# Kernel tuning notes

Measured on AMD Instinct MI355X. Metric: run time of the kernel, lower is better.

Reference implementation:

```python
import jax, jax.numpy as jnp
import numpy as np

D = 256          # object_dim == query_dim
HG = 1024        # g hidden / output width
HF0, HF1 = 1024, 512
OUT_F = 256
N = 32768        # number of objects


def _mlp_g(h, W0, b0, W1, b1, W2, b2):
    # g=True: ReLU after every layer, including output.
    h = jax.nn.relu(h @ W0 + b0)
    h = jax.nn.relu(h @ W1 + b1)
    return jax.nn.relu(h @ W2 + b2)


def _mlp_f(h, W0, b0, W1, b1, W2, b2):
    # f: ReLU on hidden layers, linear output.
    h = jax.nn.relu(h @ W0 + b0)
    h = jax.nn.relu(h @ W1 + b1)
    return h @ W2 + b2


def setup_inputs() -> dict:
    key = jax.random.key(0)
    ks = jax.random.split(key, 16)
    def lin(k, fan_in, fan_out):
        s = 1.0 / np.sqrt(fan_in)
        kw, kb = jax.random.split(k)
        W = jax.random.uniform(kw, (fan_in, fan_out), jnp.float32, -s, s)
        b = jax.random.uniform(kb, (fan_out,), jnp.float32, -s, s)
        return W, b
    x = jax.random.normal(ks[0], (N, D), jnp.float32)
    q = jax.random.normal(ks[1], (D,), jnp.float32)
    g_W0, g_b0 = lin(ks[2], 3 * D, HG)
    g_W1, g_b1 = lin(ks[3], HG, HG)
    g_W2, g_b2 = lin(ks[4], HG, HG)
    f_W0, f_b0 = lin(ks[5], HG, HF0)
    f_W1, f_b1 = lin(ks[6], HF0, HF1)
    f_W2, f_b2 = lin(ks[7], HF1, OUT_F)
    return dict(x=x, q=q,
                g_W0=g_W0, g_b0=g_b0, g_W1=g_W1, g_b1=g_b1, g_W2=g_W2, g_b2=g_b2,
                f_W0=f_W0, f_b0=f_b0, f_W1=f_W1, f_b1=f_b1, f_W2=f_W2, f_b2=f_b2)


def reference(x, q, g_W0, g_b0, g_W1, g_b1, g_W2, g_b2,
              f_W0, f_b0, f_W1, f_b1, f_W2, f_b2):
    n = x.shape[0]
    # mode 4: adjacent pairs (o_i, o_{i+1}), query concatenated to each pair.
    pair_concat = jnp.concatenate(
        [x[:-1], x[1:], jnp.broadcast_to(q, (n - 1, q.shape[0]))], axis=-1)  # (n-1, 3D)
    relations = _mlp_g(pair_concat, g_W0, g_b0, g_W1, g_b1, g_W2, g_b2)       # (n-1, HG)
    embedding = jnp.sum(relations, axis=0)                                     # (HG,)
    return _mlp_f(embedding, f_W0, f_b0, f_W1, f_b1, f_W2, f_b2)               # (OUT_F,)
```

## Files before the change

kernel.cpp:

```cpp
#include <hip/hip_runtime.h>

typedef __attribute__((ext_vector_type(8))) short short8;
typedef __attribute__((ext_vector_type(4))) float floatx4;
typedef __attribute__((ext_vector_type(4))) unsigned int uint32x4;

#define NROWS 32768L
#define NVALID 32767L
#define HGDIM 1024

__device__ __forceinline__ unsigned short f2bf_rne(float f) {
    union { float f; unsigned u; } v; v.f = f;
    unsigned r = v.u + 0x7fffu + ((v.u >> 16) & 1u);
    return (unsigned short)(r >> 16);
}

__device__ __forceinline__ void gload_lds16(const void* g, void* l) {
    __builtin_amdgcn_global_load_lds(
        (const __attribute__((address_space(1))) void*)g,
        (__attribute__((address_space(3))) void*)l,
        16, 0, 0);
}

#define NB_CVT 8193
#define NB_T0  512
#define NB_T1  1024
#define NB_T2  1024
#define NB_C0  4

__global__ void prep(const float* __restrict__ x, unsigned short* __restrict__ xb,
                     const float* __restrict__ gW0, unsigned short* __restrict__ w0t,
                     const float* __restrict__ gW1, unsigned short* __restrict__ w1t,
                     const float* __restrict__ gW2, unsigned short* __restrict__ w2t,
                     const float* __restrict__ q, const float* __restrict__ gb0,
                     float* __restrict__ c0, float* __restrict__ emb,
                     float* __restrict__ e1, float* __restrict__ e2,
                     float* __restrict__ out) {
    __shared__ float smem[1056];
    int b = blockIdx.x, tid = threadIdx.x;
    if (b < NB_CVT) {
        long i = (long)b * 256 + tid;
        long ntot4 = (NROWS + 1) * 64;
        if (i < ntot4) {
            long i4 = i * 4, nx = NROWS * 256;
            float4 v = make_float4(0.f, 0.f, 0.f, 0.f);
            if (i4 < nx) v = *(const float4*)(x + i4);
            ushort4 o;
            o.x = f2bf_rne(v.x); o.y = f2bf_rne(v.y);
            o.z = f2bf_rne(v.z); o.w = f2bf_rne(v.w);
            *(ushort4*)(xb + i4) = o;
        }
        return;
    }
    b -= NB_CVT;
    const float* W; unsigned short* Wt; int K, N;
    if (b < NB_T0)                  { W = gW0; Wt = w0t; K = 512;  N = 1024; }
    else if (b < NB_T0 + NB_T1)     { b -= NB_T0; W = gW1; Wt = w1t; K = 1024; N = 1024; }
    else if (b < NB_T0 + NB_T1 + NB_T2) { b -= NB_T0 + NB_T1; W = gW2; Wt = w2t; K = 1024; N = 1024; }
    else if (b < NB_T0 + NB_T1 + NB_T2 + NB_C0) {
        b -= NB_T0 + NB_T1 + NB_T2;
        int j = b * 256 + tid;
        smem[tid] = q[tid];
        __syncthreads();
        float a = gb0[j];
        #pragma unroll 4
        for (int k = 0; k < 256; ++k)
            a += smem[k] * gW0[(size_t)(512 + k) * 1024 + j];
        c0[j] = a;
        return;
    } else {
        for (int i = tid; i < 1024; i += 256) { emb[i] = 0.f; e1[i] = 0.f; e2[i] = 0.f; }
        if (tid < 256) out[tid] = 0.f;
        return;
    }
    int bx = b & 31, by = b >> 5;
    float (*tile)[33] = (float(*)[33])smem;
    int tx = tid & 31, ty = tid >> 5;
    int nb2 = bx * 32, kb = by * 32;
    #pragma unroll
    for (int i = 0; i < 32; i += 8)
        tile[ty + i][tx] = W[(size_t)(kb + ty + i) * N + (nb2 + tx)];
    __syncthreads();
    #pragma unroll
    for (int i = 0; i < 32; i += 8)
        Wt[(size_t)(nb2 + ty + i) * K + (kb + tx)] = f2bf_rne(tile[tx][ty + i]);
}

template<bool RELU_IN>
__global__ void fc_partial(const float* __restrict__ in, const float* __restrict__ W,
                           const float* __restrict__ bias, float* __restrict__ out,
                           int N) {
    __shared__ float s_in[128];
    int j = blockIdx.x * 256 + threadIdx.x;
    int k0 = blockIdx.y * 128;
    if (threadIdx.x < 128) {
        float v = in[k0 + threadIdx.x];
        if (RELU_IN) v = fmaxf(v, 0.f);
        s_in[threadIdx.x] = v;
    }
    __syncthreads();
    float acc = (blockIdx.y == 0) ? bias[j] : 0.f;
    #pragma unroll 4
    for (int k = 0; k < 128; ++k)
        acc += s_in[k] * W[(size_t)(k0 + k) * N + j];
    atomicAdd(&out[j], acc);
}


#define SBAR() __builtin_amdgcn_sched_barrier(0)

#define U_PRE() do { SBAR(); \
    asm volatile("s_waitcnt lgkmcnt(0)" ::: "memory"); SBAR(); \
    __builtin_amdgcn_s_setprio(1); } while (0)

#define U_POST() do { __builtin_amdgcn_s_setprio(0); SBAR(); \
    asm volatile("s_waitcnt vmcnt(2)" ::: "memory"); SBAR(); \
    __builtin_amdgcn_s_barrier(); } while (0)

#define STAGE(buf, region, T) do { \
    if ((region) >= 2) { \
        const unsigned short* _g = gA + (long)(((region) & 1) * 128) * lda + (long)(T) * 64; \
        char* _d = (char*)&lds[buf][0][((region) & 1) * 128][0] + t * 16; \
        gload_lds16(_g, _d); \
        gload_lds16(_g + 64L * lda, _d + 8192); \
    } else { \
        const unsigned short* _g = gB + (long)(((region) & 1) * 128) * ldb + (long)(T) * 64; \
        char* _d = (char*)&lds[buf][1][((region) & 1) * 128][0] + t * 16; \
        gload_lds16(_g, _d); \
        gload_lds16(_g + 64L * ldb, _d + 8192); \
    } } while (0)

#define LDA4(dst, buf, mbase, ks) do { _Pragma("unroll") for (int _q = 0; _q < 4; ++_q) \
    dst[_q] = *(const short8*)((const char*)&lds[buf][0][arowb + ((mbase) + _q) * 16][0] + ((ks) ? cb1 : cb0)); } while (0)

#define LDB4(dst, buf, ks) do { _Pragma("unroll") for (int _q = 0; _q < 4; ++_q) \
    dst[_q] = *(const short8*)((const char*)&lds[buf][1][browb + _q * 16][0] + ((ks) ? cb1 : cb0)); } while (0)

#define MFMA16(AF, BF, MO) do { _Pragma("unroll") for (int _mf = 0; _mf < 4; ++_mf) { \
    _Pragma("unroll") for (int _nf = 0; _nf < 4; ++_nf) \
        acc[(MO) + _mf][_nf] = __builtin_amdgcn_mfma_f32_16x16x32_bf16(AF[_mf], BF[_nf], acc[(MO) + _mf][_nf], 0, 0, 0); } } while (0)

template<int COLSUM>
__global__ __launch_bounds__(512, 2)
void gemmU(const unsigned short* __restrict__ A, int lda,
           const unsigned short* __restrict__ Bt, int ldb,
           const float* __restrict__ bias, int K,
           unsigned short* __restrict__ Hout,
           float* __restrict__ emb, long row0g, long nvalid,
           int mblocks) {
    __shared__ alignas(16) unsigned short lds[2][2][256][64];

    const int t = threadIdx.x;
    int nwg = gridDim.x, bid = blockIdx.x, swz;
    if ((nwg & 7) == 0) { int cpx = nwg >> 3; swz = (bid & 7) * cpx + (bid >> 3); }
    else swz = bid;
    const int mb = swz >> 2, nb = swz & 3;
    const long m0 = (long)mb * 256;
    const int n0 = nb * 256;

    const int srow = t >> 3;
    const int ssc = (t & 7) ^ (srow & 7);
    const unsigned short* gA = A + (m0 + srow) * (long)lda + ssc * 8;
    const unsigned short* gB = Bt + ((long)n0 + srow) * (long)ldb + ssc * 8;

    const int lane = t & 63;
    const int wv = t >> 6;
    const int wm = wv >> 2, wn = wv & 3;
    const int arowb = wm * 128 + (lane & 15);
    const int browb = wn * 64 + (lane & 15);
    const int c0x = (lane >> 4) ^ (lane & 7);
    const int cb0 = c0x * 16;
    const int cb1 = (c0x ^ 4) * 16;

    floatx4 acc[8][4] = {};

    const int NT = K >> 6;
    const int NI = NT >> 1;

    short8 bE0[4], bE1[4], bO0[4], bO1[4];
    short8 aE0[4], aE1[4], aE2[4], aE3[4], aO0[4], aO1[4], aO2[4], aO3[4];

    STAGE(0, 0, 0); STAGE(0, 1, 0); STAGE(0, 2, 0); STAGE(0, 3, 0);
    STAGE(1, 0, 1); STAGE(1, 1, 1);
    asm volatile("s_waitcnt vmcnt(4)" ::: "memory");
    SBAR();
    __builtin_amdgcn_s_barrier();
    SBAR();
    LDB4(bE0, 0, 0); LDA4(aE0, 0, 0, 0);

    for (int i = 0; i < NI; ++i) {
        const int O = 2 * i + 1;
        int N2 = 2 * i + 2; if (N2 >= NT) N2 = 0;
        int P2 = 2 * i + 3; if (P2 >= NT) P2 = 1;

        U_PRE();
        LDA4(aE1, 0, 4, 0);
        STAGE(1, 2, O);
        MFMA16(aE0, bE0, 0);
        U_POST();
        U_PRE();
        LDB4(bE1, 0, 1); LDA4(aE2, 0, 0, 1);
        STAGE(1, 3, O);
        MFMA16(aE1, bE0, 4);
        U_POST();
        U_PRE();
        LDA4(aE3, 0, 4, 1);
        STAGE(0, 0, N2);
        MFMA16(aE2, bE1, 0);
        U_POST();
        U_PRE();
        LDB4(bO0, 1, 0); LDA4(aO0, 1, 0, 0);
        STAGE(0, 1, N2);
        MFMA16(aE3, bE1, 4);
        U_POST();
        U_PRE();
        LDA4(aO1, 1, 4, 0);
        STAGE(0, 2, N2);
        MFMA16(aO0, bO0, 0);
        U_POST();
        U_PRE();
        LDB4(bO1, 1, 1); LDA4(aO2, 1, 0, 1);
        STAGE(0, 3, N2);
        MFMA16(aO1, bO0, 4);
        U_POST();
        U_PRE();
        LDA4(aO3, 1, 4, 1);
        STAGE(1, 0, P2);
        MFMA16(aO2, bO1, 0);
        U_POST();
        U_PRE();
        LDB4(bE0, 0, 0); LDA4(aE0, 0, 0, 0);
        STAGE(1, 1, P2);
        MFMA16(aO3, bO1, 4);
        U_POST();
    }
    asm volatile("s_waitcnt vmcnt(0) lgkmcnt(0)" ::: "memory");
    SBAR();
    __builtin_amdgcn_s_barrier();

    if (COLSUM == 0) {
        char* slb = (char*)&lds[0][0][0][0];
        #pragma unroll
        for (int nf = 0; nf < 4; ++nf) {
            int ncol = wn * 64 + nf * 16 + (lane & 15);
            float bv = bias[n0 + ncol];
            #pragma unroll
            for (int mf = 0; mf < 8; ++mf) {
                int rbase = wm * 128 + mf * 16 + ((lane >> 4) << 2);
                #pragma unroll
                for (int j = 0; j < 4; ++j) {
                    int row = rbase + j;
                    float v = fmaxf(acc[mf][nf][j] + bv, 0.f);
                    int byte = row * 512 + ((ncol * 2) ^ ((row & 7) << 4));
                    *(unsigned short*)(slb + byte) = f2bf_rne(v);
                }
            }
        }
        __syncthreads();
        {
            int rsub = t >> 5;
            int cb = (t & 31) * 16;
            #pragma unroll
            for (int i2 = 0; i2 < 16; ++i2) {
                int row = i2 * 16 + rsub;
                const char* src = slb + row * 512 + (cb ^ ((row & 7) << 4));
                uint32x4 v = *(const uint32x4*)src;
                char* dst = (char*)Hout + ((size_t)(m0 + row) * HGDIM + n0) * 2 + cb;
                *(uint32x4*)dst = v;
            }
        }
    } else {
        #pragma unroll
        for (int nf = 0; nf < 4; ++nf) {
            int ncol = n0 + wn * 64 + nf * 16 + (lane & 15);
            float bv = bias[ncol];
            float cs = 0.f;
            #pragma unroll
            for (int mf = 0; mf < 8; ++mf) {
                long rbase = row0g + m0 + wm * 128 + mf * 16 + ((lane >> 4) << 2);
                #pragma unroll
                for (int j = 0; j < 4; ++j) {
                    float v = fmaxf(acc[mf][nf][j] + bv, 0.f);
                    if (rbase + j < nvalid) cs += v;
                }
            }
            cs += __shfl_xor(cs, 16);
            cs += __shfl_xor(cs, 32);
            if ((lane >> 4) == 0) atomicAdd(&emb[ncol], cs);
        }
    }
}

extern "C" void kernel_launch(void* const* d_in, const int* in_sizes, int n_in,
                              void* d_out, int out_size, void* d_ws, size_t ws_size,
                              hipStream_t stream) {
    const float* x   = (const float*)d_in[0];
    const float* q   = (const float*)d_in[1];
    const float* gW0 = (const float*)d_in[2];
    const float* gb0 = (const float*)d_in[3];
    const float* gW1 = (const float*)d_in[4];
    const float* gb1 = (const float*)d_in[5];
    const float* gW2 = (const float*)d_in[6];
    const float* gb2 = (const float*)d_in[7];
    const float* fW0 = (const float*)d_in[8];
    const float* fb0 = (const float*)d_in[9];
    const float* fW1 = (const float*)d_in[10];
    const float* fb1 = (const float*)d_in[11];
    const float* fW2 = (const float*)d_in[12];
    const float* fb2 = (const float*)d_in[13];
    float* out = (float*)d_out;

    char* ws = (char*)d_ws;
    size_t off = 0;
    auto alloc = [&](size_t bytes) -> char* {
        char* p = ws + off;
        off += (bytes + 255) & ~(size_t)255;
        return p;
    };
    unsigned short* xb  = (unsigned short*)alloc((NROWS + 1) * 256 * 2);
    unsigned short* w0t = (unsigned short*)alloc((size_t)1024 * 512 * 2);
    unsigned short* w1t = (unsigned short*)alloc((size_t)1024 * 1024 * 2);
    unsigned short* w2t = (unsigned short*)alloc((size_t)1024 * 1024 * 2);
    float* c0  = (float*)alloc(4096);
    float* emb = (float*)alloc(4096);
    float* e1  = (float*)alloc(4096);
    float* e2  = (float*)alloc(4096);
    size_t fixed = off;
    size_t avail = (ws_size > fixed) ? ws_size - fixed : 0;
    long CR = (long)((avail / 2) / (HGDIM * 2));
    CR = (CR / 512) * 512;
    if (CR > NROWS) CR = NROWS;
    if (CR < 512) CR = 512;
    unsigned short* H0 = (unsigned short*)alloc((size_t)CR * HGDIM * 2);
    unsigned short* H1 = (unsigned short*)alloc((size_t)CR * HGDIM * 2);

    prep<<<dim3(NB_CVT + NB_T0 + NB_T1 + NB_T2 + NB_C0 + 1), 256, 0, stream>>>(
        x, xb, gW0, w0t, gW1, w1t, gW2, w2t, q, gb0, c0, emb, e1, e2, out);

    for (long r0 = 0; r0 < NROWS; r0 += CR) {
        long rows = NROWS - r0; if (rows > CR) rows = CR;
        int mblocks = (int)(rows / 256);
        dim3 g((unsigned)(mblocks * 4));
        gemmU<0><<<g, 512, 0, stream>>>(xb + r0 * 256, 256, w0t, 512, c0, 512,
                                        H0, nullptr, 0, 0, mblocks);
        gemmU<0><<<g, 512, 0, stream>>>(H0, 1024, w1t, 1024, gb1, 1024,
                                        H1, nullptr, 0, 0, mblocks);
        gemmU<1><<<g, 512, 0, stream>>>(H1, 1024, w2t, 1024, gb2, 1024,
                                        nullptr, emb, r0, NVALID, mblocks);
    }

    fc_partial<false><<<dim3(4, 8), 256, 0, stream>>>(emb, fW0, fb0, e1, 1024);
    fc_partial<true><<<dim3(2, 8), 256, 0, stream>>>(e1, fW1, fb1, e2, 512);
    fc_partial<true><<<dim3(1, 4), 256, 0, stream>>>(e2, fW2, fb2, out, 256);
}
```

Measured before the change: 234.2 us.

## Fuse prep, three GEMMs and FC layers into one cooperative persistent kernel

Replaces the sequence of separate launches (prep, three GEMMs, three FC kernels) with a single cooperative kernel of 256 workgroups. Phases are separated by grid.sync, and each workgroup processes two 256-row tiles per GEMM stage. The aim is to remove launch gaps and kernel-boundary drains. In exchange, each GEMM phase runs exactly 256 workgroups, which may fill the CUs less evenly, and grid-wide barriers add their own cost. The fused path only runs when cooperative launch is supported and the workspace holds all rows; otherwise the old multi-launch path is used.

```diff
diff --git a/kernel.cpp b/kernel.cpp
--- a/kernel.cpp
+++ b/kernel.cpp
@@ -1,4 +1,7 @@
 #include <hip/hip_runtime.h>
+#include <hip/hip_cooperative_groups.h>
+
+namespace cg = cooperative_groups;
 
 typedef __attribute__((ext_vector_type(8))) short short8;
 typedef __attribute__((ext_vector_type(4))) float floatx4;
@@ -19,6 +22,309 @@
         (const __attribute__((address_space(1))) void*)g,
         (__attribute__((address_space(3))) void*)l,
         16, 0, 0);
+}
+
+#define SBAR() __builtin_amdgcn_sched_barrier(0)
+
+#define U_PRE() do { SBAR(); \
+    asm volatile("s_waitcnt lgkmcnt(0)" ::: "memory"); SBAR(); \
+    __builtin_amdgcn_s_setprio(1); } while (0)
+
+#define U_POST() do { __builtin_amdgcn_s_setprio(0); SBAR(); \
+    asm volatile("s_waitcnt vmcnt(2)" ::: "memory"); SBAR(); \
+    __builtin_amdgcn_s_barrier(); } while (0)
+
+#define STAGE(buf, region, T) do { \
+    if ((region) >= 2) { \
+        const unsigned short* _g = gA + (long)(((region) & 1) * 128) * lda + (long)(T) * 64; \
+        char* _d = (char*)&lds[buf][0][((region) & 1) * 128][0] + t * 16; \
+        gload_lds16(_g, _d); \
+        gload_lds16(_g + 64L * lda, _d + 8192); \
+    } else { \
+        const unsigned short* _g = gB + (long)(((region) & 1) * 128) * ldb + (long)(T) * 64; \
+        char* _d = (char*)&lds[buf][1][((region) & 1) * 128][0] + t * 16; \
+        gload_lds16(_g, _d); \
+        gload_lds16(_g + 64L * ldb, _d + 8192); \
+    } } while (0)
+
+#define LDA4(dst, buf, mbase, ks) do { _Pragma("unroll") for (int _q = 0; _q < 4; ++_q) \
+    dst[_q] = *(const short8*)((const char*)&lds[buf][0][arowb + ((mbase) + _q) * 16][0] + ((ks) ? cb1 : cb0)); } while (0)
+
+#define LDB4(dst, buf, ks) do { _Pragma("unroll") for (int _q = 0; _q < 4; ++_q) \
+    dst[_q] = *(const short8*)((const char*)&lds[buf][1][browb + _q * 16][0] + ((ks) ? cb1 : cb0)); } while (0)
+
+#define MFMA16(AF, BF, MO) do { _Pragma("unroll") for (int _mf = 0; _mf < 4; ++_mf) { \
+    _Pragma("unroll") for (int _nf = 0; _nf < 4; ++_nf) \
+        acc[(MO) + _mf][_nf] = __builtin_amdgcn_mfma_f32_16x16x32_bf16(AF[_mf], BF[_nf], acc[(MO) + _mf][_nf], 0, 0, 0); } } while (0)
+
+template<int COLSUM>
+__device__ __forceinline__ void gemm_body(
+    unsigned short (&lds)[2][2][256][64],
+    const unsigned short* __restrict__ A, int lda,
+    const unsigned short* __restrict__ Bt, int ldb,
+    const float* __restrict__ bias, int K,
+    unsigned short* __restrict__ Hout, float* __restrict__ emb,
+    long row0g, long m0, int n0, long nvalid, int t)
+{
+    __syncthreads();
+
+    const int srow = t >> 3;
+    const int ssc = (t & 7) ^ (srow & 7);
+    const unsigned short* gA = A + (m0 + srow) * (long)lda + ssc * 8;
+    const unsigned short* gB = Bt + ((long)n0 + srow) * (long)ldb + ssc * 8;
+
+    const int lane = t & 63;
+    const int wv = t >> 6;
+    const int wm = wv >> 2, wn = wv & 3;
+    const int arowb = wm * 128 + (lane & 15);
+    const int browb = wn * 64 + (lane & 15);
+    const int c0x = (lane >> 4) ^ (lane & 7);
+    const int cb0 = c0x * 16;
+    const int cb1 = (c0x ^ 4) * 16;
+
+    floatx4 acc[8][4] = {};
+    const int NT = K >> 6;
+    const int NI = NT >> 1;
+
+    short8 bE0[4], bE1[4], bO0[4], bO1[4];
+    short8 aE0[4], aE1[4], aE2[4], aE3[4], aO0[4], aO1[4], aO2[4], aO3[4];
+
+    STAGE(0, 0, 0); STAGE(0, 1, 0); STAGE(0, 2, 0); STAGE(0, 3, 0);
+    STAGE(1, 0, 1); STAGE(1, 1, 1);
+    asm volatile("s_waitcnt vmcnt(4)" ::: "memory");
+    SBAR();
+    __builtin_amdgcn_s_barrier();
+    SBAR();
+    LDB4(bE0, 0, 0); LDA4(aE0, 0, 0, 0);
+
+    for (int i = 0; i < NI; ++i) {
+        const int O = 2 * i + 1;
+        int N2 = 2 * i + 2; if (N2 >= NT) N2 = 0;
+        int P2 = 2 * i + 3; if (P2 >= NT) P2 = 1;
+
+        U_PRE();
+        LDA4(aE1, 0, 4, 0);
+        STAGE(1, 2, O);
+        MFMA16(aE0, bE0, 0);
+        U_POST();
+        U_PRE();
+        LDB4(bE1, 0, 1); LDA4(aE2, 0, 0, 1);
+        STAGE(1, 3, O);
+        MFMA16(aE1, bE0, 4);
+        U_POST();
+        U_PRE();
+        LDA4(aE3, 0, 4, 1);
+        STAGE(0, 0, N2);
+        MFMA16(aE2, bE1, 0);
+        U_POST();
+        U_PRE();
+        LDB4(bO0, 1, 0); LDA4(aO0, 1, 0, 0);
+        STAGE(0, 1, N2);
+        MFMA16(aE3, bE1, 4);
+        U_POST();
+        U_PRE();
+        LDA4(aO1, 1, 4, 0);
+        STAGE(0, 2, N2);
+        MFMA16(aO0, bO0, 0);
+        U_POST();
+        U_PRE();
+        LDB4(bO1, 1, 1); LDA4(aO2, 1, 0, 1);
+        STAGE(0, 3, N2);
+        MFMA16(aO1, bO0, 4);
+        U_POST();
+        U_PRE();
+        LDA4(aO3, 1, 4, 1);
+        STAGE(1, 0, P2);
+        MFMA16(aO2, bO1, 0);
+        U_POST();
+        U_PRE();
+        LDB4(bE0, 0, 0); LDA4(aE0, 0, 0, 0);
+        STAGE(1, 1, P2);
+        MFMA16(aO3, bO1, 4);
+        U_POST();
+    }
+    asm volatile("s_waitcnt vmcnt(0) lgkmcnt(0)" ::: "memory");
+    SBAR();
+    __builtin_amdgcn_s_barrier();
+
+    if (COLSUM == 0) {
+        char* slb = (char*)&lds[0][0][0][0];
+        #pragma unroll
+        for (int nf = 0; nf < 4; ++nf) {
+            int ncol = wn * 64 + nf * 16 + (lane & 15);
+            float bv = bias[n0 + ncol];
+            #pragma unroll
+            for (int mf = 0; mf < 8; ++mf) {
+                int rbase = wm * 128 + mf * 16 + ((lane >> 4) << 2);
+                #pragma unroll
+                for (int j = 0; j < 4; ++j) {
+                    int row = rbase + j;
+                    float v = fmaxf(acc[mf][nf][j] + bv, 0.f);
+                    int byte = row * 512 + ((ncol * 2) ^ ((row & 7) << 4));
+                    *(unsigned short*)(slb + byte) = f2bf_rne(v);
+                }
+            }
+        }
+        __syncthreads();
+        {
+            int rsub = t >> 5;
+            int cb = (t & 31) * 16;
+            #pragma unroll
+            for (int i2 = 0; i2 < 16; ++i2) {
+                int row = i2 * 16 + rsub;
+                const char* src = slb + row * 512 + (cb ^ ((row & 7) << 4));
+                uint32x4 v = *(const uint32x4*)src;
+                char* dst = (char*)Hout + ((size_t)(m0 + row) * HGDIM + n0) * 2 + cb;
+                *(uint32x4*)dst = v;
+            }
+        }
+    } else {
+        #pragma unroll
+        for (int nf = 0; nf < 4; ++nf) {
+            int ncol = n0 + wn * 64 + nf * 16 + (lane & 15);
+            float bv = bias[ncol];
+            float cs = 0.f;
+            #pragma unroll
+            for (int mf = 0; mf < 8; ++mf) {
+                long rbase = row0g + m0 + wm * 128 + mf * 16 + ((lane >> 4) << 2);
+                #pragma unroll
+                for (int j = 0; j < 4; ++j) {
+                    float v = fmaxf(acc[mf][nf][j] + bv, 0.f);
+                    if (rbase + j < nvalid) cs += v;
+                }
+            }
+            cs += __shfl_xor(cs, 16);
+            cs += __shfl_xor(cs, 32);
+            if ((lane >> 4) == 0) atomicAdd(&emb[ncol], cs);
+        }
+    }
+}
+
+struct RNParams {
+    const float *x, *q, *gW0, *gb0, *gW1, *gb1, *gW2, *gb2;
+    const float *fW0, *fb0, *fW1, *fb1, *fW2, *fb2;
+    unsigned short *xb, *w0t, *w1t, *w2t;
+    float *c0, *emb, *e1, *e2;
+    unsigned short *H0, *H1;
+    float *outp;
+};
+
+__device__ __forceinline__ void fc_phase(bool relu_in, const float* in, const float* W,
+                                         const float* bias, float* out, int N, int ky,
+                                         int t, int bid, float* sbuf) {
+    int nx = N >> 8;
+    int njobs = nx * ky;
+    bool act = bid < njobs;
+    int bx = 0, by = 0;
+    if (act) { bx = bid % nx; by = bid / nx; }
+    if (act && t < 128) {
+        float v = in[by * 128 + t];
+        if (relu_in) v = fmaxf(v, 0.f);
+        sbuf[t] = v;
+    }
+    __syncthreads();
+    if (act && t < 256) {
+        int j = bx * 256 + t;
+        float a = (by == 0) ? bias[j] : 0.f;
+        #pragma unroll 4
+        for (int k = 0; k < 128; ++k)
+            a += sbuf[k] * W[(size_t)(by * 128 + k) * N + j];
+        atomicAdd(&out[j], a);
+    }
+    __syncthreads();
+}
+
+__global__ __launch_bounds__(512, 2) void fused_rn(RNParams p) {
+    __shared__ alignas(16) unsigned short lds[2][2][256][64];
+    cg::grid_group grid = cg::this_grid();
+    const int bid = blockIdx.x, t = threadIdx.x;
+
+    {
+        long ntot4 = (NROWS + 1) * 64;
+        long nx = NROWS * 256;
+        for (long i = (long)bid * 512 + t; i < ntot4; i += 131072) {
+            long i4 = i * 4;
+            float4 v = make_float4(0.f, 0.f, 0.f, 0.f);
+            if (i4 < nx) v = *(const float4*)(p.x + i4);
+            ushort4 o;
+            o.x = f2bf_rne(v.x); o.y = f2bf_rne(v.y);
+            o.z = f2bf_rne(v.z); o.w = f2bf_rne(v.w);
+            *(ushort4*)(p.xb + i4) = o;
+        }
+    }
+    {
+        float (*tiles)[32][33] = (float (*)[32][33])((void*)lds);
+        int half = t >> 8, ht = t & 255;
+        int tx = ht & 31, ty = ht >> 5;
+        for (int job = bid * 2 + half; job < 2560; job += 512) {
+            const float* W; unsigned short* Wt; int K, N; int jj = job;
+            if (jj < 512)       {             W = p.gW0; Wt = p.w0t; K = 512;  N = 1024; }
+            else if (jj < 1536) { jj -= 512;  W = p.gW1; Wt = p.w1t; K = 1024; N = 1024; }
+            else                { jj -= 1536; W = p.gW2; Wt = p.w2t; K = 1024; N = 1024; }
+            int bx = jj & 31, by = jj >> 5;
+            int nb2 = bx * 32, kb = by * 32;
+            #pragma unroll
+            for (int i = 0; i < 32; i += 8)
+                tiles[half][ty + i][tx] = W[(size_t)(kb + ty + i) * N + (nb2 + tx)];
+            __syncthreads();
+            #pragma unroll
+            for (int i = 0; i < 32; i += 8)
+                Wt[(size_t)(nb2 + ty + i) * K + (kb + tx)] = f2bf_rne(tiles[half][tx][ty + i]);
+            __syncthreads();
+        }
+    }
+    {
+        float* qs = (float*)lds;
+        if (bid < 4 && t < 256) qs[t] = p.q[t];
+        __syncthreads();
+        if (bid < 4 && t < 256) {
+            int j = bid * 256 + t;
+            float a = p.gb0[j];
+            #pragma unroll 4
+            for (int k = 0; k < 256; ++k)
+                a += qs[k] * p.gW0[(size_t)(512 + k) * 1024 + j];
+            p.c0[j] = a;
+        } else if (bid == 4) {
+            for (int i2 = t; i2 < 1024; i2 += 512) { p.emb[i2] = 0.f; p.e1[i2] = 0.f; p.e2[i2] = 0.f; }
+            if (t < 256) p.outp[t] = 0.f;
+        }
+    }
+    __threadfence();
+    grid.sync();
+
+    int swz = (bid & 7) * 32 + (bid >> 3);
+    const int mbB = swz >> 2, nb = swz & 3;
+    const long m0a = (long)mbB * 512;
+    const int n0 = nb * 256;
+
+    #pragma clang loop unroll(disable)
+    for (int s = 0; s < 2; ++s)
+        gemm_body<0>(lds, p.xb, 256, p.w0t, 512, p.c0, 512, p.H0, nullptr,
+                     0, m0a + s * 256, n0, 0, t);
+    __threadfence();
+    grid.sync();
+
+    #pragma clang loop unroll(disable)
+    for (int s = 0; s < 2; ++s)
+        gemm_body<0>(lds, p.H0, 1024, p.w1t, 1024, p.gb1, 1024, p.H1, nullptr,
+                     0, m0a + s * 256, n0, 0, t);
+    __threadfence();
+    grid.sync();
+
+    #pragma clang loop unroll(disable)
+    for (int s = 0; s < 2; ++s)
+        gemm_body<1>(lds, p.H1, 1024, p.w2t, 1024, p.gb2, 1024, nullptr, p.emb,
+                     0, m0a + s * 256, n0, NVALID, t);
+    __threadfence();
+    grid.sync();
+
+    fc_phase(false, p.emb, p.fW0, p.fb0, p.e1, 1024, 8, t, bid, (float*)lds);
+    __threadfence();
+    grid.sync();
+    fc_phase(true, p.e1, p.fW1, p.fb1, p.e2, 512, 8, t, bid, (float*)lds);
+    __threadfence();
+    grid.sync();
+    fc_phase(true, p.e2, p.fW2, p.fb2, p.outp, 256, 4, t, bid, (float*)lds);
 }
 
 #define NB_CVT 8193
@@ -105,189 +411,20 @@
     atomicAdd(&out[j], acc);
 }
 
-
-#define SBAR() __builtin_amdgcn_sched_barrier(0)
-
-#define U_PRE() do { SBAR(); \
-    asm volatile("s_waitcnt lgkmcnt(0)" ::: "memory"); SBAR(); \
-    __builtin_amdgcn_s_setprio(1); } while (0)
-
-#define U_POST() do { __builtin_amdgcn_s_setprio(0); SBAR(); \
-    asm volatile("s_waitcnt vmcnt(2)" ::: "memory"); SBAR(); \
-    __builtin_amdgcn_s_barrier(); } while (0)
-
-#define STAGE(buf, region, T) do { \
-    if ((region) >= 2) { \
-        const unsigned short* _g = gA + (long)(((region) & 1) * 128) * lda + (long)(T) * 64; \
-        char* _d = (char*)&lds[buf][0][((region) & 1) * 128][0] + t * 16; \
-        gload_lds16(_g, _d); \
-        gload_lds16(_g + 64L * lda, _d + 8192); \
-    } else { \
-        const unsigned short* _g = gB + (long)(((region) & 1) * 128) * ldb + (long)(T) * 64; \
-        char* _d = (char*)&lds[buf][1][((region) & 1) * 128][0] + t * 16; \
-        gload_lds16(_g, _d); \
-        gload_lds16(_g + 64L * ldb, _d + 8192); \
-    } } while (0)
-
-#define LDA4(dst, buf, mbase, ks) do { _Pragma("unroll") for (int _q = 0; _q < 4; ++_q) \
-    dst[_q] = *(const short8*)((const char*)&lds[buf][0][arowb + ((mbase) + _q) * 16][0] + ((ks) ? cb1 : cb0)); } while (0)
-
-#define LDB4(dst, buf, ks) do { _Pragma("unroll") for (int _q = 0; _q < 4; ++_q) \
-    dst[_q] = *(const short8*)((const char*)&lds[buf][1][browb + _q * 16][0] + ((ks) ? cb1 : cb0)); } while (0)
-
-#define MFMA16(AF, BF, MO) do { _Pragma("unroll") for (int _mf = 0; _mf < 4; ++_mf) { \
-    _Pragma("unroll") for (int _nf = 0; _nf < 4; ++_nf) \
-        acc[(MO) + _mf][_nf] = __builtin_amdgcn_mfma_f32_16x16x32_bf16(AF[_mf], BF[_nf], acc[(MO) + _mf][_nf], 0, 0, 0); } } while (0)
-
 template<int COLSUM>
 __global__ __launch_bounds__(512, 2)
-void gemmU(const unsigned short* __restrict__ A, int lda,
-           const unsigned short* __restrict__ Bt, int ldb,
-           const float* __restrict__ bias, int K,
-           unsigned short* __restrict__ Hout,
-           float* __restrict__ emb, long row0g, long nvalid,
-           int mblocks) {
+void gemm_k(const unsigned short* __restrict__ A, int lda,
+            const unsigned short* __restrict__ Bt, int ldb,
+            const float* __restrict__ bias, int K,
+            unsigned short* __restrict__ Hout, float* __restrict__ emb,
+            long row0g, long nvalid) {
     __shared__ alignas(16) unsigned short lds[2][2][256][64];
-
-    const int t = threadIdx.x;
     int nwg = gridDim.x, bid = blockIdx.x, swz;
     if ((nwg & 7) == 0) { int cpx = nwg >> 3; swz = (bid & 7) * cpx + (bid >> 3); }
     else swz = bid;
-    const int mb = swz >> 2, nb = swz & 3;
-    const long m0 = (long)mb * 256;
-    const int n0 = nb * 256;
-
-    const int srow = t >> 3;
-    const int ssc = (t & 7) ^ (srow & 7);
-    const unsigned short* gA = A + (m0 + srow) * (long)lda + ssc * 8;
-    const unsigned short* gB = Bt + ((long)n0 + srow) * (long)ldb + ssc * 8;
-
-    const int lane = t & 63;
-    const int wv = t >> 6;
-    const int wm = wv >> 2, wn = wv & 3;
-    const int arowb = wm * 128 + (lane & 15);
-    const int browb = wn * 64 + (lane & 15);
-    const int c0x = (lane >> 4) ^ (lane & 7);
-    const int cb0 = c0x * 16;
-    const int cb1 = (c0x ^ 4) * 16;
-
-    floatx4 acc[8][4] = {};
-
-    const int NT = K >> 6;
-    const int NI = NT >> 1;
-
-    short8 bE0[4], bE1[4], bO0[4], bO1[4];
-    short8 aE0[4], aE1[4], aE2[4], aE3[4], aO0[4], aO1[4], aO2[4], aO3[4];
-
-    STAGE(0, 0, 0); STAGE(0, 1, 0); STAGE(0, 2, 0); STAGE(0, 3, 0);
-    STAGE(1, 0, 1); STAGE(1, 1, 1);
-    asm volatile("s_waitcnt vmcnt(4)" ::: "memory");
-    SBAR();
-    __builtin_amdgcn_s_barrier();
-    SBAR();
-    LDB4(bE0, 0, 0); LDA4(aE0, 0, 0, 0);
-
-    for (int i = 0; i < NI; ++i) {
-        const int O = 2 * i + 1;
-        int N2 = 2 * i + 2; if (N2 >= NT) N2 = 0;
-        int P2 = 2 * i + 3; if (P2 >= NT) P2 = 1;
-
-        U_PRE();
-        LDA4(aE1, 0, 4, 0);
-        STAGE(1, 2, O);
-        MFMA16(aE0, bE0, 0);
-        U_POST();
-        U_PRE();
-        LDB4(bE1, 0, 1); LDA4(aE2, 0, 0, 1);
-        STAGE(1, 3, O);
-        MFMA16(aE1, bE0, 4);
-        U_POST();
-        U_PRE();
-        LDA4(aE3, 0, 4, 1);
-        STAGE(0, 0, N2);
-        MFMA16(aE2, bE1, 0);
-        U_POST();
-        U_PRE();
-        LDB4(bO0, 1, 0); LDA4(aO0, 1, 0, 0);
-        STAGE(0, 1, N2);
-        MFMA16(aE3, bE1, 4);
-        U_POST();
-        U_PRE();
-        LDA4(aO1, 1, 4, 0);
-        STAGE(0, 2, N2);
-        MFMA16(aO0, bO0, 0);
-        U_POST();
-        U_PRE();
-        LDB4(bO1, 1, 1); LDA4(aO2, 1, 0, 1);
-        STAGE(0, 3, N2);
-        MFMA16(aO1, bO0, 4);
-        U_POST();
-        U_PRE();
-        LDA4(aO3, 1, 4, 1);
-        STAGE(1, 0, P2);
-        MFMA16(aO2, bO1, 0);
-        U_POST();
-        U_PRE();
-        LDB4(bE0, 0, 0); LDA4(aE0, 0, 0, 0);
-        STAGE(1, 1, P2);
-        MFMA16(aO3, bO1, 4);
-        U_POST();
-    }
-    asm volatile("s_waitcnt vmcnt(0) lgkmcnt(0)" ::: "memory");
-    SBAR();
-    __builtin_amdgcn_s_barrier();
-
-    if (COLSUM == 0) {
-        char* slb = (char*)&lds[0][0][0][0];
-        #pragma unroll
-        for (int nf = 0; nf < 4; ++nf) {
-            int ncol = wn * 64 + nf * 16 + (lane & 15);
-            float bv = bias[n0 + ncol];
-            #pragma unroll
-            for (int mf = 0; mf < 8; ++mf) {
-                int rbase = wm * 128 + mf * 16 + ((lane >> 4) << 2);
-                #pragma unroll
-                for (int j = 0; j < 4; ++j) {
-                    int row = rbase + j;
-                    float v = fmaxf(acc[mf][nf][j] + bv, 0.f);
-                    int byte = row * 512 + ((ncol * 2) ^ ((row & 7) << 4));
-                    *(unsigned short*)(slb + byte) = f2bf_rne(v);
-                }
-            }
-        }
-        __syncthreads();
-        {
-            int rsub = t >> 5;
-            int cb = (t & 31) * 16;
-            #pragma unroll
-            for (int i2 = 0; i2 < 16; ++i2) {
-                int row = i2 * 16 + rsub;
-                const char* src = slb + row * 512 + (cb ^ ((row & 7) << 4));
-                uint32x4 v = *(const uint32x4*)src;
-                char* dst = (char*)Hout + ((size_t)(m0 + row) * HGDIM + n0) * 2 + cb;
-                *(uint32x4*)dst = v;
-            }
-        }
-    } else {
-        #pragma unroll
-        for (int nf = 0; nf < 4; ++nf) {
-            int ncol = n0 + wn * 64 + nf * 16 + (lane & 15);
-            float bv = bias[ncol];
-            float cs = 0.f;
-            #pragma unroll
-            for (int mf = 0; mf < 8; ++mf) {
-                long rbase = row0g + m0 + wm * 128 + mf * 16 + ((lane >> 4) << 2);
-                #pragma unroll
-                for (int j = 0; j < 4; ++j) {
-                    float v = fmaxf(acc[mf][nf][j] + bv, 0.f);
-                    if (rbase + j < nvalid) cs += v;
-                }
-            }
-            cs += __shfl_xor(cs, 16);
-            cs += __shfl_xor(cs, 32);
-            if ((lane >> 4) == 0) atomicAdd(&emb[ncol], cs);
-        }
-    }
+    int mb = swz >> 2, nb = swz & 3;
+    gemm_body<COLSUM>(lds, A, lda, Bt, ldb, bias, K, Hout, emb,
+                      row0g, (long)mb * 256, nb * 256, nvalid, threadIdx.x);
 }
 
 extern "C" void kernel_launch(void* const* d_in, const int* in_sizes, int n_in,
@@ -333,22 +470,38 @@
     unsigned short* H0 = (unsigned short*)alloc((size_t)CR * HGDIM * 2);
     unsigned short* H1 = (unsigned short*)alloc((size_t)CR * HGDIM * 2);
 
-    prep<<<dim3(NB_CVT + NB_T0 + NB_T1 + NB_T2 + NB_C0 + 1), 256, 0, stream>>>(
-        x, xb, gW0, w0t, gW1, w1t, gW2, w2t, q, gb0, c0, emb, e1, e2, out);
-
-    for (long r0 = 0; r0 < NROWS; r0 += CR) {
-        long rows = NROWS - r0; if (rows > CR) rows = CR;
-        int mblocks = (int)(rows / 256);
-        dim3 g((unsigned)(mblocks * 4));
-        gemmU<0><<<g, 512, 0, stream>>>(xb + r0 * 256, 256, w0t, 512, c0, 512,
-                                        H0, nullptr, 0, 0, mblocks);
-        gemmU<0><<<g, 512, 0, stream>>>(H0, 1024, w1t, 1024, gb1, 1024,
-                                        H1, nullptr, 0, 0, mblocks);
-        gemmU<1><<<g, 512, 0, stream>>>(H1, 1024, w2t, 1024, gb2, 1024,
-                                        nullptr, emb, r0, NVALID, mblocks);
-    }
-
-    fc_partial<false><<<dim3(4, 8), 256, 0, stream>>>(emb, fW0, fb0, e1, 1024);
-    fc_partial<true><<<dim3(2, 8), 256, 0, stream>>>(e1, fW1, fb1, e2, 512);
-    fc_partial<true><<<dim3(1, 4), 256, 0, stream>>>(e2, fW2, fb2, out, 256);
-}
+    int dev = 0;
+    hipGetDevice(&dev);
+    int coop = 0;
+    hipDeviceGetAttribute(&coop, hipDeviceAttributeCooperativeLaunch, dev);
+
+    if (coop && CR >= NROWS) {
+        RNParams p;
+        p.x = x; p.q = q; p.gW0 = gW0; p.gb0 = gb0; p.gW1 = gW1; p.gb1 = gb1;
+        p.gW2 = gW2; p.gb2 = gb2; p.fW0 = fW0; p.fb0 = fb0; p.fW1 = fW1; p.fb1 = fb1;
+        p.fW2 = fW2; p.fb2 = fb2; p.xb = xb; p.w0t = w0t; p.w1t = w1t; p.w2t = w2t;
+        p.c0 = c0; p.emb = emb; p.e1 = e1; p.e2 = e2; p.H0 = H0; p.H1 = H1; p.outp = out;
+        void* kargs[] = { (void*)&p };
+        hipLaunchCooperativeKernel((const void*)fused_rn, dim3(256), dim3(512),
+                                   kargs, 0, stream);
+    } else {
+        prep<<<dim3(NB_CVT + NB_T0 + NB_T1 + NB_T2 + NB_C0 + 1), 256, 0, stream>>>(
+            x, xb, gW0, w0t, gW1, w1t, gW2, w2t, q, gb0, c0, emb, e1, e2, out);
+
+        for (long r0 = 0; r0 < NROWS; r0 += CR) {
+            long rows = NROWS - r0; if (rows > CR) rows = CR;
+            int mblocks = (int)(rows / 256);
+            dim3 g((unsigned)(mblocks * 4));
+            gemm_k<0><<<g, 512, 0, stream>>>(xb + r0 * 256, 256, w0t, 512, c0, 512,
+                                             H0, nullptr, 0, 0);
+            gemm_k<0><<<g, 512, 0, stream>>>(H0, 1024, w1t, 1024, gb1, 1024,
+                                             H1, nullptr, 0, 0);
+            gemm_k<1><<<g, 512, 0, stream>>>(H1, 1024, w2t, 1024, gb2, 1024,
+                                             nullptr, emb, r0, NVALID);
+        }
+
+        fc_partial<false><<<dim3(4, 8), 256, 0, stream>>>(emb, fW0, fb0, e1, 1024);
+        fc_partial<true><<<dim3(2, 8), 256, 0, stream>>>(e1, fW1, fb1, e2, 512);
+        fc_partial<true><<<dim3(1, 4), 256, 0, stream>>>(e2, fW2, fb2, out, 256);
+    }
+}
```

Result: slower. 762.5 us (+225.6%).
